# Kernel optimization log

Measured on AMD Instinct MI355X. Metric: run time of the kernel, lower is better.

The kernel has to match this reference:

```python
import jax, jax.numpy as jnp
import numpy as np

_EPS = 1e-5
RC = 5.0   # cutoff radius
L = 20     # number of radial basis functions
N = 10000  # nodes
E = 100000 # edges
F = 128    # in_feats


def _ssp(x):
    # ShiftedSoftplus: softplus(x) - log(2)
    return jax.nn.softplus(x) - jnp.log(2.0)


def _rbf(r):
    # DimeNet radial basis: sqrt(2/rc) * sin(n*pi*r/rc) / r, n = 1..L.  r: [E,1] -> [E,L]
    n = jnp.arange(1, L + 1, dtype=r.dtype)
    return jnp.sqrt(2.0 / RC) * jnp.sin(n * jnp.pi * r / RC) / r


def _fc(u):
    # cosine cutoff applied elementwise: 0.5*(cos(pi*u/rc)+1) for u < rc else 0
    return jnp.where(u < RC, 0.5 * (jnp.cos(jnp.pi * u / RC) + 1.0), 0.0)


def setup_inputs() -> dict:
    key = jax.random.key(0)
    ks = jax.random.split(key, 12)

    def nrm(k, shape, scale=1.0):
        return jax.random.normal(k, shape, dtype=jnp.float32) * scale

    return {
        "x": nrm(ks[0], (N, 3)) * 3.0,           # atomic positions
        "v": nrm(ks[1], (N, F, 3)),               # vector node features
        "s": nrm(ks[2], (N, F)),                  # scalar node features
        "ms1_w": nrm(ks[3], (F, F), F ** -0.5),
        "ms1_b": jnp.zeros((F,), jnp.float32),
        "ms2_w": nrm(ks[4], (3 * F, F), F ** -0.5),
        "ms2_b": jnp.zeros((3 * F,), jnp.float32),
        "mv_w": nrm(ks[5], (3 * F, L), L ** -0.5),
        "mv_b": jnp.zeros((3 * F,), jnp.float32),
        "us1_w": nrm(ks[6], (F, F), F ** -0.5),
        "us1_b": jnp.zeros((F,), jnp.float32),
        "us2_w": nrm(ks[7], (3 * F, F), F ** -0.5),
        "us2_b": jnp.zeros((3 * F,), jnp.float32),
        "src": jax.random.randint(ks[8], (E,), 0, N, dtype=jnp.int32),
        "dst": jax.random.randint(ks[9], (E,), 0, N, dtype=jnp.int32),
    }


def reference(x, v, s, ms1_w, ms1_b, ms2_w, ms2_b, mv_w, mv_b,
              us1_w, us1_b, us2_w, us2_b, src, dst):
    # ---------- pass 1: message1 + reduce1 (sum over incoming edges) ----------
    sj = s[src]                                   # [E,F]   src scalar features
    vj = v[src]                                   # [E,F,3] src vector features
    vec = x[src] - x[dst]                         # [E,3]   x_i - x_j (molecule branch)
    r = jnp.sqrt(jnp.sum(vec ** 2, axis=-1) + _EPS)[:, None]          # [E,1]
    phi = _ssp(sj @ ms1_w.T + ms1_b) @ ms2_w.T + ms2_b                 # [E,3F]
    w = _fc(_rbf(r) @ mv_w.T + mv_b)                                    # [E,3F]
    v_, s_, r_ = jnp.split(phi * w, 3, axis=-1)                         # each [E,F]
    dv_e = vj * v_[:, :, None] + r_[:, :, None] * (vec / r)[:, None, :] # [E,F,3]
    dv = jax.ops.segment_sum(dv_e, dst, num_segments=N)                 # [N,F,3]
    ds = jax.ops.segment_sum(s_, dst, num_segments=N)                   # [N,F]
    v_new = v + dv
    s_new = s + ds

    # ---------- pass 2: message2 + reduce2 (mean over incoming edges) ----------
    s2 = _ssp(s_new[src] @ us1_w.T + us1_b) @ us2_w.T + us2_b           # [E,3F]
    deg = jax.ops.segment_sum(jnp.ones((E,), s.dtype), dst, num_segments=N)
    denom = jnp.maximum(deg, 1.0)
    s_mean = jax.ops.segment_sum(s2, dst, num_segments=N) / denom[:, None]        # [N,3F]
    uv = jax.ops.segment_sum(v_new[src], dst, num_segments=N) / denom[:, None, None]  # [N,F,3]
    avv, asv, ass = jnp.split(s_mean, 3, axis=-1)                       # each [N,F]
    norm = jnp.sqrt(jnp.sum(uv ** 2, axis=-1) + _EPS)[..., None]        # [N,F,1]
    dv2 = uv * avv[:, :, None]                                           # [N,F,3]
    ds2 = jnp.sum((uv / norm) ** 2, axis=-1) * asv + ass                 # [N,F]
    return (v_new + dv2, s_new + ds2)
```

## Files before the change

### kernel.cpp

```cpp
#include <hip/hip_runtime.h>
#include <hip/hip_bf16.h>


#define F_DIM   128
#define F3_DIM  384
#define L_DIM   20
#define CAP     64
#define BATCH   16

typedef __attribute__((ext_vector_type(8))) short short8;
typedef __attribute__((ext_vector_type(4))) float f32x4;
typedef __attribute__((ext_vector_type(4))) unsigned short us4;

struct u3 { unsigned a, b, c; };

__device__ __forceinline__ unsigned short f2bf(float f) {
  union { float f; unsigned u; } a; a.f = f;
  unsigned u = a.u;
  u = (u + 0x7FFFu + ((u >> 16) & 1u)) >> 16;
  return (unsigned short)u;
}
__device__ __forceinline__ float bf2f(unsigned short u) {
  union { unsigned u; float f; } a; a.u = ((unsigned)u) << 16;
  return a.f;
}

__global__ __launch_bounds__(256) void cast_fill_kernel(
    const float* __restrict__ ms1_w, unsigned short* __restrict__ w_ms1,
    const float* __restrict__ ms2_w, unsigned short* __restrict__ w_ms2,
    const float* __restrict__ us1_w, unsigned short* __restrict__ w_us1,
    const float* __restrict__ us2_w, unsigned short* __restrict__ w_us2,
    const float* __restrict__ s,     unsigned short* __restrict__ sbf,
    const float* __restrict__ mv_w,  unsigned short* __restrict__ mvwB,
    const int* __restrict__ src, const int* __restrict__ dst,
    int* __restrict__ cursor, int* __restrict__ jbuf,
    unsigned short* __restrict__ c1pad, unsigned short* __restrict__ v4pad,
    int nF, int E)
{
  int i = blockIdx.x * 256 + threadIdx.x;
  if (i < 16384) w_ms1[i] = f2bf(ms1_w[i]);
  if (i < 49152) w_ms2[i] = f2bf(ms2_w[i]);
  if (i < 16384) w_us1[i] = f2bf(us1_w[i]);
  if (i < 49152) w_us2[i] = f2bf(us2_w[i]);
  if (i < nF)    sbf[i] = f2bf(s[i]);
  if (i < 384 * 32) {
    int o = i >> 5, k = i & 31;
    float val = (k < 20) ? mv_w[o * 20 + k] * 0.6324555320336759f : 0.f;
    mvwB[i] = f2bf(val);
  }
  if (i < 768) c1pad[i] = 0;
  if (i < 512) v4pad[i] = 0;
  if (i < E) {
    int d = dst[i];
    int p = atomicAdd(&cursor[d], 1);
    if (p < CAP) jbuf[d * CAP + p] = src[i];
  }
}

__global__ __launch_bounds__(512) void mlp_kernel(
    const unsigned short* __restrict__ X,
    const unsigned short* __restrict__ W1,
    const float* __restrict__ B1,
    const unsigned short* __restrict__ W2,
    const float* __restrict__ B2,
    const float* __restrict__ Vfp,
    unsigned short* __restrict__ Yc)
{
  __shared__ float HT[128 * 17];
  const int lane = threadIdx.x & 63;
  const int wave = threadIdx.x >> 6;
  const int c    = lane & 15;
  const int quad = lane >> 4;
  const int m0   = blockIdx.x * 16;

  f32x4 acc = (f32x4){0.f, 0.f, 0.f, 0.f};
#pragma unroll
  for (int kk = 0; kk < 4; kk++) {
    short8 a = *(const short8*)(X + (size_t)(m0 + c) * 128 + kk * 32 + quad * 8);
    short8 b = *(const short8*)(W1 + (size_t)(wave * 16 + c) * 128 + kk * 32 + quad * 8);
    acc = __builtin_amdgcn_mfma_f32_16x16x32_bf16(a, b, acc, 0, 0, 0);
  }
  {
    int k = wave * 16 + c;
    float bias = B1[k];
#pragma unroll
    for (int r = 0; r < 4; r++) {
      float h = acc[r] + bias;
      float sp = (h > 15.f) ? h : log1pf(__expf(h));
      sp -= 0.69314718056f;
      HT[k * 17 + quad * 4 + r] = sp;
    }
  }
  __syncthreads();

  f32x4 acc2[3];
#pragma unroll
  for (int g = 0; g < 3; g++) acc2[g] = (f32x4){0.f, 0.f, 0.f, 0.f};
#pragma unroll
  for (int kk = 0; kk < 4; kk++) {
    short8 afr;
#pragma unroll
    for (int j = 0; j < 8; j++) {
      float hv = HT[(kk * 32 + quad * 8 + j) * 17 + c];
      afr[j] = (short)f2bf(hv);
    }
#pragma unroll
    for (int g = 0; g < 3; g++) {
      short8 b = *(const short8*)(W2 + (size_t)(g * 128 + wave * 16 + c) * 128 + kk * 32 + quad * 8);
      acc2[g] = __builtin_amdgcn_mfma_f32_16x16x32_bf16(afr, b, acc2[g], 0, 0, 0);
    }
  }
  {
    int f = wave * 16 + c;
    float b0 = B2[f], b1 = B2[128 + f], b2 = B2[256 + f];
#pragma unroll
    for (int r = 0; r < 4; r++) {
      int m = quad * 4 + r;
      const float* vp = Vfp + ((size_t)(m0 + m) * 128 + f) * 3;
      unsigned p0 = f2bf(acc2[0][r] + b0);
      unsigned p1 = f2bf(acc2[1][r] + b1);
      unsigned p2 = f2bf(acc2[2][r] + b2);
      u3 rec;
      rec.a = p0 | (p1 << 16);
      rec.b = p2 | ((unsigned)f2bf(vp[0]) << 16);
      rec.c = (unsigned)f2bf(vp[1]) | ((unsigned)f2bf(vp[2]) << 16);
      *(u3*)(Yc + ((size_t)(m0 + m) * 128 + f) * 6) = rec;
    }
  }
}

__global__ __launch_bounds__(512) void hidden_kernel(
    const unsigned short* __restrict__ X,
    const unsigned short* __restrict__ W1,
    const float* __restrict__ B1,
    us4* __restrict__ V4)
{
  const int lane = threadIdx.x & 63;
  const int wave = threadIdx.x >> 6;
  const int c    = lane & 15;
  const int quad = lane >> 4;
  const int m0   = blockIdx.x * 16;

  f32x4 acc = (f32x4){0.f, 0.f, 0.f, 0.f};
#pragma unroll
  for (int kk = 0; kk < 4; kk++) {
    short8 a = *(const short8*)(X + (size_t)(m0 + c) * 128 + kk * 32 + quad * 8);
    short8 b = *(const short8*)(W1 + (size_t)(wave * 16 + c) * 128 + kk * 32 + quad * 8);
    acc = __builtin_amdgcn_mfma_f32_16x16x32_bf16(a, b, acc, 0, 0, 0);
  }
  int f = wave * 16 + c;
  float bias = B1[f];
#pragma unroll
  for (int r = 0; r < 4; r++) {
    int m = m0 + quad * 4 + r;
    float h = acc[r] + bias;
    float sp = (h > 15.f) ? h : log1pf(__expf(h));
    sp -= 0.69314718056f;
    us4 rec = V4[(size_t)m * 128 + f];
    rec.w = f2bf(sp);
    V4[(size_t)m * 128 + f] = rec;
  }
}

__global__ __launch_bounds__(512, 8) void pass1_kernel(
    const float* __restrict__ x,
    const unsigned short* __restrict__ combo1,
    const float* __restrict__ v,
    const float* __restrict__ s,
    const unsigned short* __restrict__ mvwB,
    const float* __restrict__ mv_b,
    const int* __restrict__ jbuf,
    const int* __restrict__ deg,
    float* __restrict__ vnew, us4* __restrict__ vnew4,
    float* __restrict__ snew, unsigned short* __restrict__ snew_bf, int nNodes)
{
  __shared__ unsigned short Asn[BATCH * 32];
  __shared__ float4 Au[BATCH];
  __shared__ us4 Wl[BATCH * 128];
  __shared__ float red[4 * 3 * 128];

  const int tid  = threadIdx.x;
  const int wave = tid >> 6, lane = tid & 63;
  const int half = wave >> 2, split = wave & 3;
  const int i = blockIdx.x;
  const int f = lane + 64 * half;
  const int c = lane & 15, quad = lane >> 4;

  int cnt = deg[i]; if (cnt > CAP) cnt = CAP;
  const int base = i * CAP;

  short8 bfr[3]; float bias[3];
#pragma unroll
  for (int p = 0; p < 3; p++) {
    int t = wave + 8 * p;
    bfr[p]  = *(const short8*)(mvwB + (size_t)(t * 16 + c) * 32 + quad * 8);
    bias[p] = mv_b[t * 16 + c];
  }

  const float xi0 = x[i * 3], xi1 = x[i * 3 + 1], xi2 = x[i * 3 + 2];
  int jv = (lane < cnt) ? jbuf[base + lane] : nNodes;

  float accV0 = 0.f, accV1 = 0.f, accV2 = 0.f, accS = 0.f;

  for (int bs = 0; bs < cnt; bs += BATCH) {
    int bcnt = cnt - bs; if (bcnt > BATCH) bcnt = BATCH;
    __syncthreads();

    {
      int e  = tid >> 4;
      int li = tid & 15;
      int se = (e < BATCH) ? bs + e : 0;
      int j  = __shfl(jv, se);
      if (e < bcnt) {
        float d0 = x[j * 3]     - xi0;
        float d1 = x[j * 3 + 1] - xi1;
        float d2 = x[j * 3 + 2] - xi2;
        float r = sqrtf(d0 * d0 + d1 * d1 + d2 * d2 + 1e-5f);
        float invr = 1.0f / r;
        if (li == 0) Au[e] = make_float4(d0 * invr, d1 * invr, d2 * invr, invr);
        float theta = r * 0.6283185307179586f;
        Asn[e * 32 + li] = f2bf(__sinf((float)(li + 1) * theta));
        unsigned short hiv = 0;
        if (li < 4) hiv = f2bf(__sinf((float)(li + 17) * theta));
        Asn[e * 32 + 16 + li] = hiv;
      }
    }
    __syncthreads();

    {
      short8 a = *(const short8*)&Asn[c * 32 + quad * 8];
      f32x4 acc[3];
#pragma unroll
      for (int p = 0; p < 3; p++)
        acc[p] = __builtin_amdgcn_mfma_f32_16x16x32_bf16(
            a, bfr[p], (f32x4){0.f, 0.f, 0.f, 0.f}, 0, 0, 0);
#pragma unroll
      for (int r = 0; r < 4; r++) {
        int el = quad * 4 + r;
        if (el < bcnt) {
          float invr = Au[el].w;
          float wp0 = fmaf(acc[0][r], invr, bias[0]);
          float wp1 = fmaf(acc[1][r], invr, bias[1]);
          float wp2 = fmaf(acc[2][r], invr, bias[2]);
          float w0 = (wp0 < 5.f) ? 0.5f * (__cosf(wp0 * 0.6283185307179586f) + 1.f) : 0.f;
          float w1 = (wp1 < 5.f) ? 0.5f * (__cosf(wp1 * 0.6283185307179586f) + 1.f) : 0.f;
          float w2 = (wp2 < 5.f) ? 0.5f * (__cosf(wp2 * 0.6283185307179586f) + 1.f) : 0.f;
          us4 o; o.x = f2bf(w0); o.y = f2bf(w1); o.z = f2bf(w2); o.w = 0;
          Wl[el * 128 + wave * 16 + c] = o;
        }
      }
    }
    __syncthreads();

    u3 cb[4];
#pragma unroll
    for (int k = 0; k < 4; k++) {
      int j = __shfl(jv, bs + split + 4 * k);
      cb[k] = *(const u3*)(combo1 + ((size_t)j * 128 + f) * 6);
    }
#pragma unroll
    for (int k = 0; k < 4; k++) {
      int el = split + 4 * k;
      if (el < bcnt) {
        float4 u = Au[el];
        us4 wv = Wl[el * 128 + f];
        float ph0 = bf2f((unsigned short)(cb[k].a & 0xffff));
        float ph1 = bf2f((unsigned short)(cb[k].a >> 16));
        float ph2 = bf2f((unsigned short)(cb[k].b & 0xffff));
        float vx  = bf2f((unsigned short)(cb[k].b >> 16));
        float vy  = bf2f((unsigned short)(cb[k].c & 0xffff));
        float vz  = bf2f((unsigned short)(cb[k].c >> 16));
        float m0 = ph0 * bf2f(wv.x);
        float m1 = ph1 * bf2f(wv.y);
        float m2 = ph2 * bf2f(wv.z);
        accV0 = fmaf(vx, m0, fmaf(m2, u.x, accV0));
        accV1 = fmaf(vy, m0, fmaf(m2, u.y, accV1));
        accV2 = fmaf(vz, m0, fmaf(m2, u.z, accV2));
        accS += m1;
      }
    }
  }

  __syncthreads();
  if (split != 0) {
    int o = (split - 1) * 128 + f;
    red[0 * 384 + o] = accV0;
    red[1 * 384 + o] = accV1;
    red[2 * 384 + o] = accV2;
    red[3 * 384 + o] = accS;
  }
  __syncthreads();
  if (split == 0) {
#pragma unroll
    for (int q = 0; q < 3; q++) {
      int o = q * 128 + f;
      accV0 += red[0 * 384 + o];
      accV1 += red[1 * 384 + o];
      accV2 += red[2 * 384 + o];
      accS  += red[3 * 384 + o];
    }
    size_t b3 = (size_t)i * 384 + f * 3;
    float n0 = v[b3] + accV0, n1 = v[b3 + 1] + accV1, n2 = v[b3 + 2] + accV2;
    vnew[b3] = n0; vnew[b3 + 1] = n1; vnew[b3 + 2] = n2;
    us4 o; o.x = f2bf(n0); o.y = f2bf(n1); o.z = f2bf(n2); o.w = 0;
    vnew4[(size_t)i * 128 + f] = o;
    size_t b1 = (size_t)i * 128 + f;
    float sv = s[b1] + accS;
    snew[b1] = sv;
    snew_bf[b1] = f2bf(sv);
  }
}

__global__ __launch_bounds__(512, 2) void pass2_kernel(
    const us4* __restrict__ vnew4,
    const int* __restrict__ jbuf, const int* __restrict__ deg,
    const unsigned short* __restrict__ W2,
    const float* __restrict__ B2,
    const float* __restrict__ vnew,
    const float* __restrict__ snew,
    float* __restrict__ vout, float* __restrict__ sout, int nNodes)
{
  __shared__ unsigned short HMb[16][136];
  __shared__ float UV[16 * 128 * 3];

  const int tid  = threadIdx.x;
  const int wave = tid >> 6, lane = tid & 63;
  const int c    = lane & 15, quad = lane >> 4;
  const int m0   = blockIdx.x * 16;

  const int ra = 2 * wave, rb = ra + 1;
  const int na = m0 + ra, nb = m0 + rb;
  int ca = deg[na]; if (ca > CAP) ca = CAP;
  int cb = deg[nb]; if (cb > CAP) cb = CAP;
  int jva = (lane < ca) ? jbuf[na * CAP + lane] : nNodes;
  int jvb = (lane < cb) ? jbuf[nb * CAP + lane] : nNodes;

  float a0l = 0.f, a1l = 0.f, a2l = 0.f, ahl = 0.f;
  float a0h = 0.f, a1h = 0.f, a2h = 0.f, ahh = 0.f;
  float b0l = 0.f, b1l = 0.f, b2l = 0.f, bhl = 0.f;
  float b0h = 0.f, b1h = 0.f, b2h = 0.f, bhh = 0.f;

  int emax = (ca > cb) ? ca : cb;
  for (int e = 0; e < emax; e += 4) {
    us4 ral[4], rah[4], rbl[4], rbh[4];
#pragma unroll
    for (int k = 0; k < 4; k++) {
      int ja = __shfl(jva, e + k);
      int jb = __shfl(jvb, e + k);
      ral[k] = vnew4[(size_t)ja * 128 + lane];
      rah[k] = vnew4[(size_t)ja * 128 + lane + 64];
      rbl[k] = vnew4[(size_t)jb * 128 + lane];
      rbh[k] = vnew4[(size_t)jb * 128 + lane + 64];
    }
#pragma unroll
    for (int k = 0; k < 4; k++) {
      a0l += bf2f(ral[k].x); a1l += bf2f(ral[k].y);
      a2l += bf2f(ral[k].z); ahl += bf2f(ral[k].w);
      a0h += bf2f(rah[k].x); a1h += bf2f(rah[k].y);
      a2h += bf2f(rah[k].z); ahh += bf2f(rah[k].w);
      b0l += bf2f(rbl[k].x); b1l += bf2f(rbl[k].y);
      b2l += bf2f(rbl[k].z); bhl += bf2f(rbl[k].w);
      b0h += bf2f(rbh[k].x); b1h += bf2f(rbh[k].y);
      b2h += bf2f(rbh[k].z); bhh += bf2f(rbh[k].w);
    }
  }

  float dia = 1.0f / (float)(ca > 0 ? ca : 1);
  float dib = 1.0f / (float)(cb > 0 ? cb : 1);
  {
    int fl = lane, fh = lane + 64;
    UV[(ra * 128 + fl) * 3 + 0] = a0l * dia;
    UV[(ra * 128 + fl) * 3 + 1] = a1l * dia;
    UV[(ra * 128 + fl) * 3 + 2] = a2l * dia;
    UV[(ra * 128 + fh) * 3 + 0] = a0h * dia;
    UV[(ra * 128 + fh) * 3 + 1] = a1h * dia;
    UV[(ra * 128 + fh) * 3 + 2] = a2h * dia;
    UV[(rb * 128 + fl) * 3 + 0] = b0l * dib;
    UV[(rb * 128 + fl) * 3 + 1] = b1l * dib;
    UV[(rb * 128 + fl) * 3 + 2] = b2l * dib;
    UV[(rb * 128 + fh) * 3 + 0] = b0h * dib;
    UV[(rb * 128 + fh) * 3 + 1] = b1h * dib;
    UV[(rb * 128 + fh) * 3 + 2] = b2h * dib;
    HMb[ra][fl] = f2bf(ahl * dia);
    HMb[ra][fh] = f2bf(ahh * dia);
    HMb[rb][fl] = f2bf(bhl * dib);
    HMb[rb][fh] = f2bf(bhh * dib);
  }
  __syncthreads();

  f32x4 acc2[3];
#pragma unroll
  for (int g = 0; g < 3; g++) acc2[g] = (f32x4){0.f, 0.f, 0.f, 0.f};
#pragma unroll
  for (int kk = 0; kk < 4; kk++) {
    short8 afr = *(const short8*)&HMb[c][kk * 32 + quad * 8];
#pragma unroll
    for (int g = 0; g < 3; g++) {
      short8 b = *(const short8*)(W2 + (size_t)(g * 128 + wave * 16 + c) * 128 + kk * 32 + quad * 8);
      acc2[g] = __builtin_amdgcn_mfma_f32_16x16x32_bf16(afr, b, acc2[g], 0, 0, 0);
    }
  }

  int f = wave * 16 + c;
  float bb0 = B2[f], bb1 = B2[128 + f], bb2 = B2[256 + f];
#pragma unroll
  for (int r = 0; r < 4; r++) {
    int m = quad * 4 + r;
    int gm = m0 + m;
    float z = (deg[gm] > 0) ? 1.f : 0.f;
    float avv = (acc2[0][r] + bb0) * z;
    float asv = (acc2[1][r] + bb1) * z;
    float ass = (acc2[2][r] + bb2) * z;
    float uv0 = UV[(m * 128 + f) * 3 + 0];
    float uv1 = UV[(m * 128 + f) * 3 + 1];
    float uv2 = UV[(m * 128 + f) * 3 + 2];
    float q = uv0 * uv0 + uv1 * uv1 + uv2 * uv2;
    float ds2 = (q / (q + 1e-5f)) * asv + ass;
    size_t b3 = (size_t)gm * 384 + f * 3;
    vout[b3]     = vnew[b3]     + uv0 * avv;
    vout[b3 + 1] = vnew[b3 + 1] + uv1 * avv;
    vout[b3 + 2] = vnew[b3 + 2] + uv2 * avv;
    size_t b1i = (size_t)gm * 128 + f;
    sout[b1i] = snew[b1i] + ds2;
  }
}

extern "C" void kernel_launch(void* const* d_in, const int* in_sizes, int n_in,
                              void* d_out, int out_size, void* d_ws, size_t ws_size,
                              hipStream_t stream)
{
  const float* x     = (const float*)d_in[0];
  const float* v     = (const float*)d_in[1];
  const float* s     = (const float*)d_in[2];
  const float* ms1_w = (const float*)d_in[3];
  const float* ms1_b = (const float*)d_in[4];
  const float* ms2_w = (const float*)d_in[5];
  const float* ms2_b = (const float*)d_in[6];
  const float* mv_w  = (const float*)d_in[7];
  const float* mv_b  = (const float*)d_in[8];
  const float* us1_w = (const float*)d_in[9];
  const float* us1_b = (const float*)d_in[10];
  const float* us2_w = (const float*)d_in[11];
  const float* us2_b = (const float*)d_in[12];
  const int*   src   = (const int*)d_in[13];
  const int*   dst   = (const int*)d_in[14];

  const int N = in_sizes[0] / 3;
  const int E = in_sizes[13];

  char* p = (char*)d_ws;
  auto alloc = [&](size_t bytes) -> void* {
    void* r = (void*)p;
    p += (bytes + 255) & ~(size_t)255;
    return r;
  };
  unsigned short* sbf   = (unsigned short*)alloc((size_t)N * 128 * 2);
  unsigned short* snbf  = (unsigned short*)alloc((size_t)N * 128 * 2);
  unsigned short* w_ms1 = (unsigned short*)alloc(16384 * 2);
  unsigned short* w_ms2 = (unsigned short*)alloc(49152 * 2);
  unsigned short* w_us1 = (unsigned short*)alloc(16384 * 2);
  unsigned short* w_us2 = (unsigned short*)alloc(49152 * 2);
  unsigned short* mvwB  = (unsigned short*)alloc(384 * 32 * 2);
  us4*   vnew4  = (us4*)alloc((size_t)(N + 1) * 128 * 8);
  unsigned short* combo1 = (unsigned short*)alloc((size_t)(N + 1) * 128 * 12);
  float* vnew   = (float*)alloc((size_t)N * 384 * 4);
  float* snew   = (float*)alloc((size_t)N * 128 * 4);
  int* cursor   = (int*)alloc((size_t)N * 4);
  int* jbuf     = (int*)alloc((size_t)N * CAP * 4);

  hipMemsetAsync(cursor, 0, (size_t)N * 4, stream);

  cast_fill_kernel<<<(N * 128 + 255) / 256, 256, 0, stream>>>(
      ms1_w, w_ms1, ms2_w, w_ms2, us1_w, w_us1, us2_w, w_us2,
      s, sbf, mv_w, mvwB, src, dst, cursor, jbuf,
      combo1 + (size_t)N * 768, (unsigned short*)(vnew4 + (size_t)N * 128),
      N * 128, E);

  mlp_kernel<<<N / 16, 512, 0, stream>>>(sbf, w_ms1, ms1_b, w_ms2, ms2_b,
                                         v, combo1);

  pass1_kernel<<<N, 512, 0, stream>>>(x, combo1, v, s, mvwB, mv_b,
                                      jbuf, cursor, vnew, vnew4, snew, snbf, N);

  hidden_kernel<<<N / 16, 512, 0, stream>>>(snbf, w_us1, us1_b, vnew4);

  float* vout = (float*)d_out;
  float* sout = vout + (size_t)N * 384;
  pass2_kernel<<<N / 16, 512, 0, stream>>>(vnew4, jbuf, cursor, w_us2, us2_b,
                                           vnew, snew, vout, sout, N);
}
```

Baseline: 245.2 us.

## Process 16 nodes per block in pass1 with packed edge slots

Pass1 now handles 16 destination nodes per block instead of one. A prefix sum over the nodes' degrees packs all their incoming edges into 32-edge slot batches, so the RBF/MFMA stage runs on fully packed tiles. Each wave owns two nodes and accumulates all 128 features itself, which removes the cross-wave shared-memory reduction. The intent is to cut per-block launch overhead and the waste from partially filled 16-edge batches. In exchange, wave load depends on per-node degree, so waves can be imbalanced, and there is only one block per 16 nodes, which lowers the number of blocks in flight.

```diff
diff --git a/kernel.cpp b/kernel.cpp
--- a/kernel.cpp
+++ b/kernel.cpp
@@ -6,7 +6,6 @@
 #define F3_DIM  384
 #define L_DIM   20
 #define CAP     64
-#define BATCH   16
 
 typedef __attribute__((ext_vector_type(8))) short short8;
 typedef __attribute__((ext_vector_type(4))) float f32x4;
@@ -162,7 +161,7 @@
   }
 }
 
-__global__ __launch_bounds__(512, 8) void pass1_kernel(
+__global__ __launch_bounds__(512) void pass1_kernel(
     const float* __restrict__ x,
     const unsigned short* __restrict__ combo1,
     const float* __restrict__ v,
@@ -174,20 +173,39 @@
     float* __restrict__ vnew, us4* __restrict__ vnew4,
     float* __restrict__ snew, unsigned short* __restrict__ snew_bf, int nNodes)
 {
-  __shared__ unsigned short Asn[BATCH * 32];
-  __shared__ float4 Au[BATCH];
-  __shared__ us4 Wl[BATCH * 128];
-  __shared__ float red[4 * 3 * 128];
+  __shared__ int offs[17];
+  __shared__ unsigned short slotmap[16 * CAP];
+  __shared__ unsigned short Asn[32 * 32];
+  __shared__ float4 Au[32];
+  __shared__ us4 Wl[32 * 128];
 
   const int tid  = threadIdx.x;
   const int wave = tid >> 6, lane = tid & 63;
-  const int half = wave >> 2, split = wave & 3;
-  const int i = blockIdx.x;
-  const int f = lane + 64 * half;
-  const int c = lane & 15, quad = lane >> 4;
-
-  int cnt = deg[i]; if (cnt > CAP) cnt = CAP;
-  const int base = i * CAP;
+  const int c    = lane & 15, quad = lane >> 4;
+  const int m0   = blockIdx.x * 16;
+
+  if (wave == 0) {
+    int cc = 0;
+    if (lane < 16) { cc = deg[m0 + lane]; if (cc > CAP) cc = CAP; }
+    int sc = cc;
+#pragma unroll
+    for (int d = 1; d < 16; d <<= 1) {
+      int srcl = (lane >= d) ? lane - d : 0;
+      int t = __shfl(sc, srcl);
+      if (lane >= d && lane < 16) sc += t;
+    }
+    if (lane < 16) offs[lane] = sc - cc;
+    if (lane == 15) offs[16] = sc;
+  }
+  __syncthreads();
+
+  const int ra = 2 * wave, rb = ra + 1;
+  const int oa = offs[ra], ca = offs[ra + 1] - oa;
+  const int ob = offs[rb], cb = offs[rb + 1] - ob;
+  const int tot = offs[16];
+  if (lane < ca) slotmap[oa + lane] = (unsigned short)((ra << 8) | lane);
+  if (lane < cb) slotmap[ob + lane] = (unsigned short)((rb << 8) | lane);
+  __syncthreads();
 
   short8 bfr[3]; float bias[3];
 #pragma unroll
@@ -197,117 +215,160 @@
     bias[p] = mv_b[t * 16 + c];
   }
 
-  const float xi0 = x[i * 3], xi1 = x[i * 3 + 1], xi2 = x[i * 3 + 2];
-  int jv = (lane < cnt) ? jbuf[base + lane] : nNodes;
-
-  float accV0 = 0.f, accV1 = 0.f, accV2 = 0.f, accS = 0.f;
-
-  for (int bs = 0; bs < cnt; bs += BATCH) {
-    int bcnt = cnt - bs; if (bcnt > BATCH) bcnt = BATCH;
-    __syncthreads();
+  float a0l = 0.f, a1l = 0.f, a2l = 0.f, aSl = 0.f;
+  float a0h = 0.f, a1h = 0.f, a2h = 0.f, aSh = 0.f;
+  float b0l = 0.f, b1l = 0.f, b2l = 0.f, bSl = 0.f;
+  float b0h = 0.f, b1h = 0.f, b2h = 0.f, bSh = 0.f;
+
+  for (int s0 = 0; s0 < tot; s0 += 32) {
+    int scnt = tot - s0; if (scnt > 32) scnt = 32;
 
     {
-      int e  = tid >> 4;
+      int sl = tid >> 4;
       int li = tid & 15;
-      int se = (e < BATCH) ? bs + e : 0;
-      int j  = __shfl(jv, se);
-      if (e < bcnt) {
+      if (sl < scnt) {
+        int nk = slotmap[s0 + sl];
+        int n  = nk >> 8, k = nk & 255;
+        int gi = m0 + n;
+        int j  = jbuf[gi * CAP + k];
+        float xi0 = x[gi * 3], xi1 = x[gi * 3 + 1], xi2 = x[gi * 3 + 2];
         float d0 = x[j * 3]     - xi0;
         float d1 = x[j * 3 + 1] - xi1;
         float d2 = x[j * 3 + 2] - xi2;
         float r = sqrtf(d0 * d0 + d1 * d1 + d2 * d2 + 1e-5f);
         float invr = 1.0f / r;
-        if (li == 0) Au[e] = make_float4(d0 * invr, d1 * invr, d2 * invr, invr);
+        if (li == 0) Au[sl] = make_float4(d0 * invr, d1 * invr, d2 * invr, invr);
         float theta = r * 0.6283185307179586f;
-        Asn[e * 32 + li] = f2bf(__sinf((float)(li + 1) * theta));
+        Asn[sl * 32 + li] = f2bf(__sinf((float)(li + 1) * theta));
         unsigned short hiv = 0;
         if (li < 4) hiv = f2bf(__sinf((float)(li + 17) * theta));
-        Asn[e * 32 + 16 + li] = hiv;
+        Asn[sl * 32 + 16 + li] = hiv;
       }
     }
     __syncthreads();
 
-    {
-      short8 a = *(const short8*)&Asn[c * 32 + quad * 8];
-      f32x4 acc[3];
-#pragma unroll
-      for (int p = 0; p < 3; p++)
-        acc[p] = __builtin_amdgcn_mfma_f32_16x16x32_bf16(
-            a, bfr[p], (f32x4){0.f, 0.f, 0.f, 0.f}, 0, 0, 0);
-#pragma unroll
-      for (int r = 0; r < 4; r++) {
-        int el = quad * 4 + r;
-        if (el < bcnt) {
-          float invr = Au[el].w;
-          float wp0 = fmaf(acc[0][r], invr, bias[0]);
-          float wp1 = fmaf(acc[1][r], invr, bias[1]);
-          float wp2 = fmaf(acc[2][r], invr, bias[2]);
-          float w0 = (wp0 < 5.f) ? 0.5f * (__cosf(wp0 * 0.6283185307179586f) + 1.f) : 0.f;
-          float w1 = (wp1 < 5.f) ? 0.5f * (__cosf(wp1 * 0.6283185307179586f) + 1.f) : 0.f;
-          float w2 = (wp2 < 5.f) ? 0.5f * (__cosf(wp2 * 0.6283185307179586f) + 1.f) : 0.f;
-          us4 o; o.x = f2bf(w0); o.y = f2bf(w1); o.z = f2bf(w2); o.w = 0;
-          Wl[el * 128 + wave * 16 + c] = o;
+#pragma unroll
+    for (int g = 0; g < 2; g++) {
+      if (g * 16 < scnt) {
+        short8 a = *(const short8*)&Asn[(g * 16 + c) * 32 + quad * 8];
+        f32x4 acc[3];
+#pragma unroll
+        for (int p = 0; p < 3; p++)
+          acc[p] = __builtin_amdgcn_mfma_f32_16x16x32_bf16(
+              a, bfr[p], (f32x4){0.f, 0.f, 0.f, 0.f}, 0, 0, 0);
+#pragma unroll
+        for (int r = 0; r < 4; r++) {
+          int el = g * 16 + quad * 4 + r;
+          if (el < scnt) {
+            float invr = Au[el].w;
+            float wp0 = fmaf(acc[0][r], invr, bias[0]);
+            float wp1 = fmaf(acc[1][r], invr, bias[1]);
+            float wp2 = fmaf(acc[2][r], invr, bias[2]);
+            float w0 = (wp0 < 5.f) ? 0.5f * (__cosf(wp0 * 0.6283185307179586f) + 1.f) : 0.f;
+            float w1 = (wp1 < 5.f) ? 0.5f * (__cosf(wp1 * 0.6283185307179586f) + 1.f) : 0.f;
+            float w2 = (wp2 < 5.f) ? 0.5f * (__cosf(wp2 * 0.6283185307179586f) + 1.f) : 0.f;
+            us4 o; o.x = f2bf(w0); o.y = f2bf(w1); o.z = f2bf(w2); o.w = 0;
+            Wl[el * 128 + wave * 16 + c] = o;
+          }
         }
       }
     }
     __syncthreads();
 
-    u3 cb[4];
-#pragma unroll
-    for (int k = 0; k < 4; k++) {
-      int j = __shfl(jv, bs + split + 4 * k);
-      cb[k] = *(const u3*)(combo1 + ((size_t)j * 128 + f) * 6);
-    }
-#pragma unroll
-    for (int k = 0; k < 4; k++) {
-      int el = split + 4 * k;
-      if (el < bcnt) {
-        float4 u = Au[el];
-        us4 wv = Wl[el * 128 + f];
-        float ph0 = bf2f((unsigned short)(cb[k].a & 0xffff));
-        float ph1 = bf2f((unsigned short)(cb[k].a >> 16));
-        float ph2 = bf2f((unsigned short)(cb[k].b & 0xffff));
-        float vx  = bf2f((unsigned short)(cb[k].b >> 16));
-        float vy  = bf2f((unsigned short)(cb[k].c & 0xffff));
-        float vz  = bf2f((unsigned short)(cb[k].c >> 16));
-        float m0 = ph0 * bf2f(wv.x);
-        float m1 = ph1 * bf2f(wv.y);
-        float m2 = ph2 * bf2f(wv.z);
-        accV0 = fmaf(vx, m0, fmaf(m2, u.x, accV0));
-        accV1 = fmaf(vy, m0, fmaf(m2, u.y, accV1));
-        accV2 = fmaf(vz, m0, fmaf(m2, u.z, accV2));
-        accS += m1;
+#pragma unroll
+    for (int nn = 0; nn < 2; nn++) {
+      int on  = nn ? ob : oa;
+      int cn  = nn ? cb : ca;
+      int gi  = m0 + (nn ? rb : ra);
+      int lo  = (on > s0) ? on : s0;
+      int hi0 = on + cn, hi1 = s0 + scnt;
+      int hi  = (hi0 < hi1) ? hi0 : hi1;
+      for (int sg = lo; sg < hi; ++sg) {
+        int k  = sg - on;
+        int j  = jbuf[gi * CAP + k];
+        int sl = sg - s0;
+        float4 u  = Au[sl];
+        us4 wlo = Wl[sl * 128 + lane];
+        us4 whi = Wl[sl * 128 + lane + 64];
+        u3 clo = *(const u3*)(combo1 + ((size_t)j * 128 + lane) * 6);
+        u3 chi = *(const u3*)(combo1 + ((size_t)j * 128 + lane + 64) * 6);
+        {
+          float ph0 = bf2f((unsigned short)(clo.a & 0xffff));
+          float ph1 = bf2f((unsigned short)(clo.a >> 16));
+          float ph2 = bf2f((unsigned short)(clo.b & 0xffff));
+          float vx  = bf2f((unsigned short)(clo.b >> 16));
+          float vy  = bf2f((unsigned short)(clo.c & 0xffff));
+          float vz  = bf2f((unsigned short)(clo.c >> 16));
+          float mm0 = ph0 * bf2f(wlo.x);
+          float mm1 = ph1 * bf2f(wlo.y);
+          float mm2 = ph2 * bf2f(wlo.z);
+          if (nn == 0) {
+            a0l = fmaf(vx, mm0, fmaf(mm2, u.x, a0l));
+            a1l = fmaf(vy, mm0, fmaf(mm2, u.y, a1l));
+            a2l = fmaf(vz, mm0, fmaf(mm2, u.z, a2l));
+            aSl += mm1;
+          } else {
+            b0l = fmaf(vx, mm0, fmaf(mm2, u.x, b0l));
+            b1l = fmaf(vy, mm0, fmaf(mm2, u.y, b1l));
+            b2l = fmaf(vz, mm0, fmaf(mm2, u.z, b2l));
+            bSl += mm1;
+          }
+        }
+        {
+          float ph0 = bf2f((unsigned short)(chi.a & 0xffff));
+          float ph1 = bf2f((unsigned short)(chi.a >> 16));
+          float ph2 = bf2f((unsigned short)(chi.b & 0xffff));
+          float vx  = bf2f((unsigned short)(chi.b >> 16));
+          float vy  = bf2f((unsigned short)(chi.c & 0xffff));
+          float vz  = bf2f((unsigned short)(chi.c >> 16));
+          float mm0 = ph0 * bf2f(whi.x);
+          float mm1 = ph1 * bf2f(whi.y);
+          float mm2 = ph2 * bf2f(whi.z);
+          if (nn == 0) {
+            a0h = fmaf(vx, mm0, fmaf(mm2, u.x, a0h));
+            a1h = fmaf(vy, mm0, fmaf(mm2, u.y, a1h));
+            a2h = fmaf(vz, mm0, fmaf(mm2, u.z, a2h));
+            aSh += mm1;
+          } else {
+            b0h = fmaf(vx, mm0, fmaf(mm2, u.x, b0h));
+            b1h = fmaf(vy, mm0, fmaf(mm2, u.y, b1h));
+            b2h = fmaf(vz, mm0, fmaf(mm2, u.z, b2h));
+            bSh += mm1;
+          }
+        }
       }
     }
-  }
-
-  __syncthreads();
-  if (split != 0) {
-    int o = (split - 1) * 128 + f;
-    red[0 * 384 + o] = accV0;
-    red[1 * 384 + o] = accV1;
-    red[2 * 384 + o] = accV2;
-    red[3 * 384 + o] = accS;
-  }
-  __syncthreads();
-  if (split == 0) {
-#pragma unroll
-    for (int q = 0; q < 3; q++) {
-      int o = q * 128 + f;
-      accV0 += red[0 * 384 + o];
-      accV1 += red[1 * 384 + o];
-      accV2 += red[2 * 384 + o];
-      accS  += red[3 * 384 + o];
-    }
-    size_t b3 = (size_t)i * 384 + f * 3;
-    float n0 = v[b3] + accV0, n1 = v[b3 + 1] + accV1, n2 = v[b3 + 2] + accV2;
-    vnew[b3] = n0; vnew[b3 + 1] = n1; vnew[b3 + 2] = n2;
-    us4 o; o.x = f2bf(n0); o.y = f2bf(n1); o.z = f2bf(n2); o.w = 0;
-    vnew4[(size_t)i * 128 + f] = o;
-    size_t b1 = (size_t)i * 128 + f;
-    float sv = s[b1] + accS;
-    snew[b1] = sv;
-    snew_bf[b1] = f2bf(sv);
+    __syncthreads();
+  }
+
+#pragma unroll
+  for (int nn = 0; nn < 2; nn++) {
+    int gi = m0 + (nn ? rb : ra);
+    float v0l = nn ? b0l : a0l, v1l = nn ? b1l : a1l, v2l = nn ? b2l : a2l;
+    float sl_ = nn ? bSl : aSl;
+    float v0h = nn ? b0h : a0h, v1h = nn ? b1h : a1h, v2h = nn ? b2h : a2h;
+    float sh_ = nn ? bSh : aSh;
+    {
+      size_t b3 = (size_t)gi * 384 + lane * 3;
+      float n0 = v[b3] + v0l, n1 = v[b3 + 1] + v1l, n2 = v[b3 + 2] + v2l;
+      vnew[b3] = n0; vnew[b3 + 1] = n1; vnew[b3 + 2] = n2;
+      us4 o; o.x = f2bf(n0); o.y = f2bf(n1); o.z = f2bf(n2); o.w = 0;
+      vnew4[(size_t)gi * 128 + lane] = o;
+      size_t b1 = (size_t)gi * 128 + lane;
+      float sv = s[b1] + sl_;
+      snew[b1] = sv; snew_bf[b1] = f2bf(sv);
+    }
+    {
+      int f = lane + 64;
+      size_t b3 = (size_t)gi * 384 + f * 3;
+      float n0 = v[b3] + v0h, n1 = v[b3 + 1] + v1h, n2 = v[b3 + 2] + v2h;
+      vnew[b3] = n0; vnew[b3 + 1] = n1; vnew[b3 + 2] = n2;
+      us4 o; o.x = f2bf(n0); o.y = f2bf(n1); o.z = f2bf(n2); o.w = 0;
+      vnew4[(size_t)gi * 128 + f] = o;
+      size_t b1 = (size_t)gi * 128 + f;
+      float sv = s[b1] + sh_;
+      snew[b1] = sv; snew_bf[b1] = f2bf(sv);
+    }
   }
 }
 
@@ -479,8 +540,9 @@
   mlp_kernel<<<N / 16, 512, 0, stream>>>(sbf, w_ms1, ms1_b, w_ms2, ms2_b,
                                          v, combo1);
 
-  pass1_kernel<<<N, 512, 0, stream>>>(x, combo1, v, s, mvwB, mv_b,
-                                      jbuf, cursor, vnew, vnew4, snew, snbf, N);
+  pass1_kernel<<<N / 16, 512, 0, stream>>>(x, combo1, v, s, mvwB, mv_b,
+                                           jbuf, cursor, vnew, vnew4, snew,
+                                           snbf, N);
 
   hidden_kernel<<<N / 16, 512, 0, stream>>>(snbf, w_us1, us1_b, vnew4);
 
```

New measurement: 293.3 us. 1.2x slower.
